# Optimization experiments

Hardware: AMD Instinct MI355X
Metric: run time of the kernel (lower is better)

## Reference

```python
import jax, jax.numpy as jnp
import numpy as np

# dims
B, S, IN, H = 8, 2048, 512, 512
# biophysical constants (from module defaults / buffers)
DT = 0.1
TAU_M, TAU_ADAPT = 20.0, 100.0
V_REST, V_THRESH, V_RESET = -65.0, -50.0, -65.0
ADAPT_A, ADAPT_B = 0.5, 0.1
E_NA, E_K, E_L = 50.0, -77.0, -54.4
# HH gate initial values (IonicCurrents lazy init)
M0, H0, N0 = 0.05, 0.6, 0.32


def setup_inputs() -> dict:
    key = jax.random.key(0)
    k1, k2 = jax.random.split(key)
    x = jax.random.normal(k1, (B, S, IN), dtype=jnp.float32)
    W = jax.random.normal(k2, (H, IN), dtype=jnp.float32) * 0.01  # SynapticPlasticity.weights
    return {
        "x": x,
        "W": W,
        "g_Na": jnp.float32(120.0),
        "g_K": jnp.float32(36.0),
        "g_L": jnp.float32(0.3),
    }


def reference(x, W, g_Na, g_K, g_L):
    """BiologicalSNNLayer.forward, first call (all internal states at init).

    post_spikes = psp0 = 0 and traces start at 0, so the STDP dw is exactly 0
    on this call; psp = 0*decay + syn_input = syn_input.
    """
    dt = jnp.float32(DT)
    # SynapticPlasticity forward output: F.linear(x, W)
    syn = jnp.einsum("bsi,hi->bsh", x, W)  # [B,S,H]
    psp = syn
    V = psp
    # Hodgkin-Huxley gating: one Euler step from initial gate values
    am = 0.1 * (V + 40.0) / (1.0 - jnp.exp(-(V + 40.0) / 10.0))
    bm = 4.0 * jnp.exp(-(V + 65.0) / 18.0)
    ah = 0.07 * jnp.exp(-(V + 65.0) / 20.0)
    bh = 1.0 / (1.0 + jnp.exp(-(V + 35.0) / 10.0))
    an = 0.01 * (V + 55.0) / (1.0 - jnp.exp(-(V + 55.0) / 10.0))
    bn = 0.125 * jnp.exp(-(V + 65.0) / 80.0)
    m = M0 + dt * (am * (1.0 - M0) - bm * M0)
    h = H0 + dt * (ah * (1.0 - H0) - bh * H0)
    n = N0 + dt * (an * (1.0 - N0) - bn * N0)
    I_ion = (
        g_Na * m ** 3 * h * (V - E_NA)
        + g_K * n ** 4 * (V - E_K)
        + g_L * (V - E_L)
    )
    # Adaptive LIF (all hidden_size neurons share params -> vectorized over last dim)
    I_in = I_ion + psp
    # v0 = V_REST, w0 = 0 -> dv = I_in * dt/tau_m
    v_new = V_REST + I_in * (dt / TAU_M)
    spike = (v_new >= V_THRESH).astype(jnp.float32)
    w_new = (ADAPT_A * (v_new - V_REST) + ADAPT_B * spike) * (dt / TAU_ADAPT)
    v_rs = jnp.where(spike > 0.5, jnp.float32(V_RESET), v_new)
    return spike, v_rs, w_new
```

## Files before the change

### kernel.cpp

```cpp
#include <hip/hip_runtime.h>
#include <hip/hip_bf16.h>

typedef __bf16 bf16x4 __attribute__((ext_vector_type(4)));
typedef __bf16 bf16x8 __attribute__((ext_vector_type(8)));
typedef float  f32x4  __attribute__((ext_vector_type(4)));

#define BM 128
#define BN 128
#define BK 64
#define LDST 72

#define M_DIM 16384
#define N_DIM 512
#define K_DIM 512

__global__ __launch_bounds__(256, 2)
void snn_fused_kernel(const float* __restrict__ x, const float* __restrict__ W,
                      const float* __restrict__ gNa_p, const float* __restrict__ gK_p,
                      const float* __restrict__ gL_p, float* __restrict__ out)
{
    __shared__ __bf16 sA[BM * LDST];
    __shared__ __bf16 sB[BN * LDST];

    const int tid = threadIdx.x;
    const int bM  = blockIdx.y;
    const int bN  = blockIdx.x;

    const int c4 = (tid & 15) * 4;
    const int r0 = tid >> 4;

    const float* xBase = x + (long)(bM * BM + r0) * K_DIM + c4;
    const float* wBase = W + (long)(bN * BN + r0) * K_DIM + c4;

    const int wave = tid >> 6;
    const int lane = tid & 63;
    const int wM   = (wave & 1) * 64;
    const int wN   = (wave >> 1) * 64;
    const int lr   = lane & 15;
    const int quad = lane >> 4;

    f32x4 acc[4][4] = {};

    for (int kt = 0; kt < K_DIM; kt += BK) {
        const float* xp = xBase + kt;
        const float* wp = wBase + kt;
        #pragma unroll
        for (int rr = 0; rr < 8; ++rr) {
            const int row = r0 + rr * 16;
            float4 va = *(const float4*)(xp + (long)rr * 16 * K_DIM);
            float4 vb = *(const float4*)(wp + (long)rr * 16 * K_DIM);
            bf16x4 ba = { (__bf16)va.x, (__bf16)va.y, (__bf16)va.z, (__bf16)va.w };
            bf16x4 bb = { (__bf16)vb.x, (__bf16)vb.y, (__bf16)vb.z, (__bf16)vb.w };
            *(bf16x4*)(&sA[row * LDST + c4]) = ba;
            *(bf16x4*)(&sB[row * LDST + c4]) = bb;
        }
        __syncthreads();

        #pragma unroll
        for (int ks = 0; ks < BK; ks += 32) {
            bf16x8 af[4], bfr[4];
            #pragma unroll
            for (int t = 0; t < 4; ++t) {
                af[t]  = *(const bf16x8*)(&sA[(wM + t * 16 + lr) * LDST + ks + quad * 8]);
                bfr[t] = *(const bf16x8*)(&sB[(wN + t * 16 + lr) * LDST + ks + quad * 8]);
            }
            #pragma unroll
            for (int mt = 0; mt < 4; ++mt)
                #pragma unroll
                for (int nt = 0; nt < 4; ++nt)
                    acc[mt][nt] = __builtin_amdgcn_mfma_f32_16x16x32_bf16(
                        af[mt], bfr[nt], acc[mt][nt], 0, 0, 0);
        }
        __syncthreads();
    }

    const float gNa = *gNa_p, gK = *gK_p, gL = *gL_p;
    float* outS = out;
    float* outV = out + (long)M_DIM * N_DIM;
    float* outW = out + 2L * M_DIM * N_DIM;

    #pragma unroll
    for (int mt = 0; mt < 4; ++mt) {
        #pragma unroll
        for (int i = 0; i < 4; ++i) {
            const long gm = (long)bM * BM + wM + mt * 16 + quad * 4 + i;
            #pragma unroll
            for (int nt = 0; nt < 4; ++nt) {
                const int gn = bN * BN + wN + nt * 16 + lr;
                const float V = acc[mt][nt][i];

                const float vp40 = V + 40.0f;
                const float vp55 = V + 55.0f;
                const float vp65 = V + 65.0f;
                const float am = 0.1f * vp40 / (1.0f - __expf(-vp40 * 0.1f));
                const float bm = 4.0f * __expf(-vp65 * (1.0f / 18.0f));
                const float ah = 0.07f * __expf(-vp65 * 0.05f);
                const float bh = 1.0f / (1.0f + __expf(-(V + 35.0f) * 0.1f));
                const float an = 0.01f * vp55 / (1.0f - __expf(-vp55 * 0.1f));
                const float bn = 0.125f * __expf(-vp65 * 0.0125f);

                const float m = 0.05f + 0.1f * (am * 0.95f - bm * 0.05f);
                const float h = 0.60f + 0.1f * (ah * 0.40f - bh * 0.60f);
                const float n = 0.32f + 0.1f * (an * 0.68f - bn * 0.32f);

                const float m3 = m * m * m;
                const float n2 = n * n;
                const float n4 = n2 * n2;

                const float I_ion = gNa * m3 * h * (V - 50.0f)
                                  + gK * n4 * (V + 77.0f)
                                  + gL * (V + 54.4f);
                const float I_in  = I_ion + V;
                const float v_new = -65.0f + I_in * 0.005f;
                const float spike = (v_new >= -50.0f) ? 1.0f : 0.0f;
                const float w_new = (0.5f * (v_new + 65.0f) + 0.1f * spike) * 0.001f;
                const float v_rs  = (spike > 0.5f) ? -65.0f : v_new;

                const long idx = gm * N_DIM + gn;
                outS[idx] = spike;
                outV[idx] = v_rs;
                outW[idx] = w_new;
            }
        }
    }
}

extern "C" void kernel_launch(void* const* d_in, const int* in_sizes, int n_in,
                              void* d_out, int out_size, void* d_ws, size_t ws_size,
                              hipStream_t stream) {
    const float* x   = (const float*)d_in[0];
    const float* W   = (const float*)d_in[1];
    const float* gNa = (const float*)d_in[2];
    const float* gK  = (const float*)d_in[3];
    const float* gL  = (const float*)d_in[4];
    float* out = (float*)d_out;

    dim3 grid(N_DIM / BN, M_DIM / BM);
    dim3 block(256);
    hipLaunchKernelGGL(snn_fused_kernel, grid, block, 0, stream, x, W, gNa, gK, gL, out);
}
```

Before: 179.2 us.

## Prefetch next K tile into registers and remap blocks by XCD

Global loads for the next K tile are now issued into registers before the MFMA loop runs, so load latency overlaps with compute instead of stalling each iteration. The grid is also flattened and block ids are remapped so that consecutive blocks on the same XCD share M rows, which should improve L2 reuse of x across the four N tiles. The cost is 64 more VGPRs per thread, which may hurt occupancy under launch_bounds(256,2).

```diff
diff --git a/kernel.cpp b/kernel.cpp
--- a/kernel.cpp
+++ b/kernel.cpp
@@ -23,14 +23,18 @@
     __shared__ __bf16 sB[BN * LDST];
 
     const int tid = threadIdx.x;
-    const int bM  = blockIdx.y;
-    const int bN  = blockIdx.x;
+
+    const int id   = blockIdx.x;
+    const int xcd  = id & 7;
+    const int slot = id >> 3;
+    const int bm   = xcd * 16 + (slot >> 2);
+    const int bn   = slot & 3;
 
     const int c4 = (tid & 15) * 4;
     const int r0 = tid >> 4;
 
-    const float* xBase = x + (long)(bM * BM + r0) * K_DIM + c4;
-    const float* wBase = W + (long)(bN * BN + r0) * K_DIM + c4;
+    const float* xBase = x + (long)(bm * BM + r0) * K_DIM + c4;
+    const float* wBase = W + (long)(bn * BN + r0) * K_DIM + c4;
 
     const int wave = tid >> 6;
     const int lane = tid & 63;
@@ -41,18 +45,33 @@
 
     f32x4 acc[4][4] = {};
 
+    float4 pa[8], pb[8];
+    #pragma unroll
+    for (int rr = 0; rr < 8; ++rr) {
+        pa[rr] = *(const float4*)(xBase + (long)rr * 16 * K_DIM);
+        pb[rr] = *(const float4*)(wBase + (long)rr * 16 * K_DIM);
+    }
+
     for (int kt = 0; kt < K_DIM; kt += BK) {
-        const float* xp = xBase + kt;
-        const float* wp = wBase + kt;
         #pragma unroll
         for (int rr = 0; rr < 8; ++rr) {
             const int row = r0 + rr * 16;
-            float4 va = *(const float4*)(xp + (long)rr * 16 * K_DIM);
-            float4 vb = *(const float4*)(wp + (long)rr * 16 * K_DIM);
+            float4 va = pa[rr];
+            float4 vb = pb[rr];
             bf16x4 ba = { (__bf16)va.x, (__bf16)va.y, (__bf16)va.z, (__bf16)va.w };
             bf16x4 bb = { (__bf16)vb.x, (__bf16)vb.y, (__bf16)vb.z, (__bf16)vb.w };
             *(bf16x4*)(&sA[row * LDST + c4]) = ba;
             *(bf16x4*)(&sB[row * LDST + c4]) = bb;
+        }
+
+        if (kt + BK < K_DIM) {
+            const float* xp = xBase + kt + BK;
+            const float* wp = wBase + kt + BK;
+            #pragma unroll
+            for (int rr = 0; rr < 8; ++rr) {
+                pa[rr] = *(const float4*)(xp + (long)rr * 16 * K_DIM);
+                pb[rr] = *(const float4*)(wp + (long)rr * 16 * K_DIM);
+            }
         }
         __syncthreads();
 
@@ -83,25 +102,25 @@
     for (int mt = 0; mt < 4; ++mt) {
         #pragma unroll
         for (int i = 0; i < 4; ++i) {
-            const long gm = (long)bM * BM + wM + mt * 16 + quad * 4 + i;
+            const long gm = (long)bm * BM + wM + mt * 16 + quad * 4 + i;
             #pragma unroll
             for (int nt = 0; nt < 4; ++nt) {
-                const int gn = bN * BN + wN + nt * 16 + lr;
+                const int gn = bn * BN + wN + nt * 16 + lr;
                 const float V = acc[mt][nt][i];
 
                 const float vp40 = V + 40.0f;
                 const float vp55 = V + 55.0f;
                 const float vp65 = V + 65.0f;
                 const float am = 0.1f * vp40 / (1.0f - __expf(-vp40 * 0.1f));
-                const float bm = 4.0f * __expf(-vp65 * (1.0f / 18.0f));
+                const float bm_ = 4.0f * __expf(-vp65 * (1.0f / 18.0f));
                 const float ah = 0.07f * __expf(-vp65 * 0.05f);
                 const float bh = 1.0f / (1.0f + __expf(-(V + 35.0f) * 0.1f));
                 const float an = 0.01f * vp55 / (1.0f - __expf(-vp55 * 0.1f));
-                const float bn = 0.125f * __expf(-vp65 * 0.0125f);
+                const float bn_ = 0.125f * __expf(-vp65 * 0.0125f);
 
-                const float m = 0.05f + 0.1f * (am * 0.95f - bm * 0.05f);
+                const float m = 0.05f + 0.1f * (am * 0.95f - bm_ * 0.05f);
                 const float h = 0.60f + 0.1f * (ah * 0.40f - bh * 0.60f);
-                const float n = 0.32f + 0.1f * (an * 0.68f - bn * 0.32f);
+                const float n = 0.32f + 0.1f * (an * 0.68f - bn_ * 0.32f);
 
                 const float m3 = m * m * m;
                 const float n2 = n * n;
@@ -135,7 +154,7 @@
     const float* gL  = (const float*)d_in[4];
     float* out = (float*)d_out;
 
-    dim3 grid(N_DIM / BN, M_DIM / BM);
+    dim3 grid((M_DIM / BM) * (N_DIM / BN));
     dim3 block(256);
     hipLaunchKernelGGL(snn_fused_kernel, grid, block, 0, stream, x, W, gNa, gK, gL, out);
 }
```

Measured after the change: 156.7 us. 12.6% less time.
